# Performance work log

Hardware: AMD Instinct MI355X
Metric: run time of the kernel (lower is better)

## Reference

```python
import jax, jax.numpy as jnp
import numpy as np

VOCAB, HIDDEN, BATCH, T = 32000, 256, 16, 256


def setup_inputs() -> dict:
    key = jax.random.key(0)
    ks = jax.random.split(key, 8)
    s_in = 1.0 / np.sqrt(HIDDEN)  # torch nn.RNN init scale (1/sqrt(hidden))
    inputs = jax.random.randint(ks[0], (BATCH, T), 0, VOCAB)
    targets = jax.random.randint(ks[1], (BATCH, T), 0, VOCAB)
    # RNN params: torch stores W_ih as (hidden, vocab); we keep the transpose
    # (vocab, hidden) so one_hot(x) @ W_ih.T == Wih[x] (an exact gather).
    Wih = jax.random.uniform(ks[2], (VOCAB, HIDDEN), minval=-s_in, maxval=s_in)
    bih = jax.random.uniform(ks[3], (HIDDEN,), minval=-s_in, maxval=s_in)
    Whh = jax.random.uniform(ks[4], (HIDDEN, HIDDEN), minval=-s_in, maxval=s_in)
    bhh = jax.random.uniform(ks[5], (HIDDEN,), minval=-s_in, maxval=s_in)
    Wfc = jax.random.uniform(ks[6], (VOCAB, HIDDEN), minval=-s_in, maxval=s_in)
    bfc = jax.random.uniform(ks[7], (VOCAB,), minval=-s_in, maxval=s_in)
    return {"inputs": inputs, "targets": targets, "Wih": Wih, "bih": bih,
            "Whh": Whh, "bhh": bhh, "Wfc": Wfc, "bfc": bfc}


def reference(inputs, targets, Wih, bih, Whh, bhh, Wfc, bfc):
    # one_hot(inputs) @ W_ih.T + b_ih  ==  Wih[inputs] + bih (exact same math)
    xproj = Wih[inputs] + bih                      # (B, T, H)
    B = inputs.shape[0]
    h0 = jnp.zeros((B, HIDDEN), dtype=Wih.dtype)

    def step(h, xt):
        h = jnp.tanh(xt + h @ Whh.T + bhh)
        return h, h

    _, hs = jax.lax.scan(step, h0, jnp.swapaxes(xproj, 0, 1))  # (T, B, H)
    hs = jnp.swapaxes(hs, 0, 1)                    # (B, T, H)
    logits = hs @ Wfc.T + bfc                      # (B, T, V)
    logp = jax.nn.log_softmax(logits, axis=-1)
    nll = -jnp.take_along_axis(logp, targets[..., None], axis=-1)
    return jnp.mean(nll)                           # scalar cross-entropy loss
```

## Files before the change

kernel.cpp:

```cpp
#include <hip/hip_runtime.h>
#include <hip/hip_bf16.h>
#include <stdint.h>

#define VOCAB 32000
#define HID   256
#define BATCH 16
#define SEQT  256
#define ROWS  (BATCH*SEQT)

typedef __attribute__((ext_vector_type(8))) short bf16x8_t;
typedef __attribute__((ext_vector_type(4))) float f32x4_t;

__device__ __forceinline__ short f2bs(float x) {
    __hip_bfloat16 h = __float2bfloat16(x);
    return *reinterpret_cast<short*>(&h);
}
__device__ __forceinline__ bf16x8_t cvt8(float4 a, float4 b) {
    union { short s[8]; bf16x8_t v; } u;
    u.s[0] = f2bs(a.x); u.s[1] = f2bs(a.y); u.s[2] = f2bs(a.z); u.s[3] = f2bs(a.w);
    u.s[4] = f2bs(b.x); u.s[5] = f2bs(b.y); u.s[6] = f2bs(b.z); u.s[7] = f2bs(b.w);
    return u.v;
}
__device__ __forceinline__ void barrier_lds() {
    asm volatile("s_waitcnt lgkmcnt(0)\n\ts_barrier" ::: "memory");
}
__device__ __forceinline__ float tanh_exp(float x) {
    float e = __builtin_amdgcn_exp2f(x * 2.885390081777927f);
    return fmaf(-2.f, __builtin_amdgcn_rcpf(e + 1.f), 1.f);
}
__device__ __forceinline__ uint32_t pk_bf16(float lo, float hi) {
    uint32_t r;
    asm("v_cvt_pk_bf16_f32 %0, %1, %2" : "=v"(r) : "v"(lo), "v"(hi));
    return r;
}


__global__ __launch_bounds__(256) void xproj_kernel(
    const int* __restrict__ inputs,
    const float* __restrict__ Wih,
    const float* __restrict__ bih,
    const float* __restrict__ bhh,
    const float* __restrict__ Wfc,
    float* __restrict__ xp,
    float* __restrict__ S,
    __hip_bfloat16* __restrict__ Wfcb,
    int do_cvt)
{
    int idx = blockIdx.x * 256 + threadIdx.x;
    int h  = idx & 255;
    int tb = idx >> 8;
    int b  = tb & 15;
    int t  = tb >> 4;
    int id = inputs[b * SEQT + t];
    xp[idx] = Wih[(size_t)id * HID + h] + bih[h] + bhh[h];
    if (idx < ROWS) S[idx] = 0.0f;
    if (do_cvt && idx < (VOCAB * HID / 8)) {
        const float4* p = (const float4*)(Wfc + (size_t)idx * 8);
        int n  = idx >> 5;
        int c  = idx & 31;
        int ki = c >> 2;
        int lh = c & 3;
        size_t dst = (size_t)(n >> 4) * 4096 + ki * 512 + lh * 128 + (n & 15) * 8;
        *(bf16x8_t*)((short*)Wfcb + dst) = cvt8(p[0], p[1]);
    }
}

__global__ __launch_bounds__(512, 1) void rnn_kernel(
    const float* __restrict__ xp,
    const float* __restrict__ Whh,
    __hip_bfloat16* __restrict__ hs)
{
    __shared__ short hbuf[2][16][264];
    const int tid = threadIdx.x;
    const int l = tid & 63, w = tid >> 6;
    const int lr = l & 15, lh = l >> 4;
    const int cm = tid >> 5;
    const int cc = (tid & 31) * 8;
    const int n0 = w * 32 + lr * 2;
    const int cpoff = ((cc >> 5) * 512) + (((cc >> 3) & 3) * 128) + cm * 8;

    bf16x8_t bfrag[2][8];
#pragma unroll
    for (int nt = 0; nt < 2; nt++) {
#pragma unroll
        for (int ki = 0; ki < 8; ki++) {
            const float4* p = (const float4*)(Whh + (size_t)(n0 + nt) * HID + ki * 32 + lh * 8);
            bfrag[nt][ki] = cvt8(p[0], p[1]);
        }
    }
    for (int i = tid; i < 16 * 264; i += 512) ((short*)hbuf[0])[i] = 0;
    __syncthreads();

    float2 xva[4], xvb[4];
#pragma unroll
    for (int r = 0; r < 4; r++)
        xva[r] = *(const float2*)(xp + (lh * 4 + r) * HID + n0);

    auto step = [&](int SRC, int DST, float2* xv, float2* xn, int t) {
        if (t > 0) {
            bf16x8_t hv = *(const bf16x8_t*)(&hbuf[SRC][cm][cc]);
            *(bf16x8_t*)((short*)hs + (size_t)(t - 1) * 4096 + cpoff) = hv;
        }
        bf16x8_t afr[8];
#pragma unroll
        for (int ki = 0; ki < 8; ki++)
            afr[ki] = *(const bf16x8_t*)(&hbuf[SRC][lr][ki * 32 + lh * 8]);

        f32x4_t a0a = {xv[0].x, xv[1].x, xv[2].x, xv[3].x};
        f32x4_t a1a = {xv[0].y, xv[1].y, xv[2].y, xv[3].y};
        f32x4_t a0b = {0.f, 0.f, 0.f, 0.f};
        f32x4_t a1b = {0.f, 0.f, 0.f, 0.f};
#pragma unroll
        for (int ki = 0; ki < 4; ki++) {
            a0a = __builtin_amdgcn_mfma_f32_16x16x32_bf16(afr[ki],     bfrag[0][ki],     a0a, 0, 0, 0);
            a0b = __builtin_amdgcn_mfma_f32_16x16x32_bf16(afr[ki + 4], bfrag[0][ki + 4], a0b, 0, 0, 0);
            a1a = __builtin_amdgcn_mfma_f32_16x16x32_bf16(afr[ki],     bfrag[1][ki],     a1a, 0, 0, 0);
            a1b = __builtin_amdgcn_mfma_f32_16x16x32_bf16(afr[ki + 4], bfrag[1][ki + 4], a1b, 0, 0, 0);
        }

        if (t + 1 < SEQT) {
            const float* xb = xp + (size_t)(t + 1) * (BATCH * HID);
#pragma unroll
            for (int r = 0; r < 4; r++)
                xn[r] = *(const float2*)(xb + (lh * 4 + r) * HID + n0);
        }

#pragma unroll
        for (int r = 0; r < 4; r++) {
            float v0 = a0a[r] + a0b[r];
            float v1 = a1a[r] + a1b[r];
            uint32_t pk = pk_bf16(tanh_exp(v0), tanh_exp(v1));
            *(uint32_t*)(&hbuf[DST][lh * 4 + r][n0]) = pk;
        }
        barrier_lds();
    };

    for (int t = 0; t < SEQT; t += 2) {
        step(0, 1, xva, xvb, t);
        step(1, 0, xvb, xva, t + 1);
    }
    bf16x8_t hv = *(const bf16x8_t*)(&hbuf[0][cm][cc]);
    *(bf16x8_t*)((short*)hs + (size_t)(SEQT - 1) * 4096 + cpoff) = hv;
}

template <bool BF16B>
__global__ __launch_bounds__(256) void fc_kernel(
    const __hip_bfloat16* __restrict__ hsz,
    const void* __restrict__ WfcP,
    const float* __restrict__ bfc,
    const int* __restrict__ targets,
    float* __restrict__ S,
    float* __restrict__ TL)
{
    __shared__ int tgt[128];

    const int bid = blockIdx.x;
    const int xcd = bid & 7;
    const int j   = bid >> 3;
    const int m_id = j & 31;
    const int n_id = (j >> 5) * 8 + xcd;
    if (n_id >= VOCAB / 128) return;
    const int m0 = m_id * 128, n0 = n_id * 128;

    const int tid = threadIdx.x;
    const int l = tid & 63, w = tid >> 6;
    const int lr = l & 15, lh = l >> 4;
    const int wm = (w >> 1) * 64, wn = (w & 1) * 64;

    if (tid < 128) {
        int r = m0 + tid;
        tgt[tid] = targets[((r & 15) << 8) | (r >> 4)];
    }

    const short* Ab = (const short*)hsz +
        ((size_t)(m_id * 8 + (wm >> 4)) * 8) * 512 + l * 8;
    const short* Bb = (const short*)WfcP +
        ((size_t)(n_id * 8 + (wn >> 4)) * 8) * 512 + l * 8;
    const float* Bf = (const float*)WfcP;

    f32x4_t acc[4][4];
    const f32x4_t z = {0.f, 0.f, 0.f, 0.f};
#pragma unroll
    for (int i = 0; i < 4; i++)
#pragma unroll
        for (int jj = 0; jj < 4; jj++) acc[i][jj] = z;

    bf16x8_t a[2][4], b[2][4];
    auto loadA = [&](int buf, int ki) {
#pragma unroll
        for (int mt = 0; mt < 4; mt++)
            a[buf][mt] = *(const bf16x8_t*)(Ab + mt * 4096 + ki * 512);
    };
    auto loadB = [&](int buf, int ki) {
#pragma unroll
        for (int nt = 0; nt < 4; nt++) {
            if (BF16B) {
                b[buf][nt] = *(const bf16x8_t*)(Bb + nt * 4096 + ki * 512);
            } else {
                int n = n0 + wn + nt * 16 + lr;
                const float4* p = (const float4*)(Bf + (size_t)n * HID + ki * 32 + lh * 8);
                b[buf][nt] = cvt8(p[0], p[1]);
            }
        }
    };

    loadA(0, 0); loadB(0, 0);
#pragma unroll
    for (int ki = 0; ki < 8; ki++) {
        const int cur = ki & 1;
        if (ki < 7) { loadA(cur ^ 1, ki + 1); loadB(cur ^ 1, ki + 1); }
#pragma unroll
        for (int mt = 0; mt < 4; mt++)
#pragma unroll
            for (int nt = 0; nt < 4; nt++)
                acc[mt][nt] = __builtin_amdgcn_mfma_f32_16x16x32_bf16(
                    a[cur][mt], b[cur][nt], acc[mt][nt], 0, 0, 0);
    }
    __syncthreads();

    int tg[16];
#pragma unroll
    for (int i = 0; i < 16; i++)
        tg[i] = tgt[wm + (i >> 2) * 16 + lh * 4 + (i & 3)];

    float rsum[16];
#pragma unroll
    for (int i = 0; i < 16; i++) rsum[i] = 0.f;
#pragma unroll
    for (int nt = 0; nt < 4; nt++) {
        int n = n0 + wn + nt * 16 + lr;
        float bias = bfc[n];
#pragma unroll
        for (int mt = 0; mt < 4; mt++)
#pragma unroll
            for (int r = 0; r < 4; r++) {
                float v = acc[mt][nt][r] + bias;
                rsum[mt * 4 + r] += __expf(v);
                if (tg[mt * 4 + r] == n)
                    TL[m0 + wm + mt * 16 + lh * 4 + r] = v;
            }
    }
#pragma unroll
    for (int m = 1; m < 16; m <<= 1)
#pragma unroll
        for (int i = 0; i < 16; i++) rsum[i] += __shfl_xor(rsum[i], m, 64);
    if (lr == 0) {
#pragma unroll
        for (int i = 0; i < 16; i++) {
            int r = m0 + wm + (i >> 2) * 16 + lh * 4 + (i & 3);
            atomicAdd(&S[r], rsum[i]);
        }
    }
}

__global__ __launch_bounds__(256) void loss_kernel(
    const float* __restrict__ S,
    const float* __restrict__ TL,
    float* __restrict__ out)
{
    int tid = threadIdx.x;
    float p = 0.f;
    for (int i = tid; i < ROWS; i += 256) p += __logf(S[i]) - TL[i];
#pragma unroll
    for (int m = 1; m < 64; m <<= 1) p += __shfl_xor(p, m, 64);
    __shared__ float red[4];
    if ((tid & 63) == 0) red[tid >> 6] = p;
    __syncthreads();
    if (tid == 0)
        out[0] = (red[0] + red[1] + red[2] + red[3]) / (float)ROWS;
}

extern "C" void kernel_launch(void* const* d_in, const int* in_sizes, int n_in,
                              void* d_out, int out_size, void* d_ws, size_t ws_size,
                              hipStream_t stream)
{
    (void)in_sizes; (void)n_in; (void)out_size;
    const int*   inputs  = (const int*)d_in[0];
    const int*   targets = (const int*)d_in[1];
    const float* Wih = (const float*)d_in[2];
    const float* bih = (const float*)d_in[3];
    const float* Whh = (const float*)d_in[4];
    const float* bhh = (const float*)d_in[5];
    const float* Wfc = (const float*)d_in[6];
    const float* bfc = (const float*)d_in[7];

    float* S  = (float*)d_ws;
    float* TL = S + ROWS;
    float* xp = TL + ROWS;
    __hip_bfloat16* hs = (__hip_bfloat16*)(xp + (size_t)SEQT * BATCH * HID);
    __hip_bfloat16* Wfcb = hs + (size_t)ROWS * HID;

    const size_t need = (size_t)(2 * ROWS) * 4 + (size_t)ROWS * HID * 4
                      + (size_t)ROWS * HID * 2 + (size_t)VOCAB * HID * 2;
    const int use_bf16b = (ws_size >= need) ? 1 : 0;

    xproj_kernel<<<(SEQT * BATCH * HID) / 256, 256, 0, stream>>>(
        inputs, Wih, bih, bhh, Wfc, xp, S, Wfcb, use_bf16b);
    rnn_kernel<<<1, 512, 0, stream>>>(xp, Whh, hs);
    if (use_bf16b)
        fc_kernel<true><<<8192, 256, 0, stream>>>(hs, (const void*)Wfcb, bfc, targets, S, TL);
    else
        fc_kernel<false><<<8192, 256, 0, stream>>>(hs, (const void*)Wfc, bfc, targets, S, TL);
    loss_kernel<<<1, 256, 0, stream>>>(S, TL, (float*)d_out);
}
```

Baseline: 468.0 us.

## Persist A tile in LDS across vocab tiles; shrink RNN to 4 waves with direct hs stores

```diff
diff --git a/kernel.cpp b/kernel.cpp
--- a/kernel.cpp
+++ b/kernel.cpp
@@ -55,96 +55,98 @@
     xp[idx] = Wih[(size_t)id * HID + h] + bih[h] + bhh[h];
     if (idx < ROWS) S[idx] = 0.0f;
     if (do_cvt && idx < (VOCAB * HID / 8)) {
-        const float4* p = (const float4*)(Wfc + (size_t)idx * 8);
-        int n  = idx >> 5;
-        int c  = idx & 31;
-        int ki = c >> 2;
-        int lh = c & 3;
-        size_t dst = (size_t)(n >> 4) * 4096 + ki * 512 + lh * 128 + (n & 15) * 8;
-        *(bf16x8_t*)((short*)Wfcb + dst) = cvt8(p[0], p[1]);
-    }
-}
-
-__global__ __launch_bounds__(512, 1) void rnn_kernel(
+        int e   = idx * 8;
+        int m   = (e >> 3) & 15;
+        int lhh = (e >> 7) & 3;
+        int ki  = (e >> 9) & 7;
+        int tile = e >> 12;
+        const float4* p = (const float4*)(Wfc + (size_t)(tile * 16 + m) * HID
+                                          + ki * 32 + lhh * 8);
+        *(bf16x8_t*)((short*)Wfcb + (size_t)e) = cvt8(p[0], p[1]);
+    }
+}
+
+__global__ __launch_bounds__(256, 1) void rnn_kernel(
     const float* __restrict__ xp,
     const float* __restrict__ Whh,
     __hip_bfloat16* __restrict__ hs)
 {
-    __shared__ short hbuf[2][16][264];
+    __shared__ __align__(16) short hbuf[2][16][264];
     const int tid = threadIdx.x;
     const int l = tid & 63, w = tid >> 6;
     const int lr = l & 15, lh = l >> 4;
-    const int cm = tid >> 5;
-    const int cc = (tid & 31) * 8;
-    const int n0 = w * 32 + lr * 2;
-    const int cpoff = ((cc >> 5) * 512) + (((cc >> 3) & 3) * 128) + cm * 8;
-
-    bf16x8_t bfrag[2][8];
-#pragma unroll
-    for (int nt = 0; nt < 2; nt++) {
+    const int n0 = w * 64 + lr * 4;
+    short* hsg = (short*)hs + ((n0 >> 5) * 512) + (((n0 >> 3) & 3) * 128) + (n0 & 7);
+
+    bf16x8_t bfrag[4][8];
+#pragma unroll
+    for (int c = 0; c < 4; c++)
 #pragma unroll
         for (int ki = 0; ki < 8; ki++) {
-            const float4* p = (const float4*)(Whh + (size_t)(n0 + nt) * HID + ki * 32 + lh * 8);
-            bfrag[nt][ki] = cvt8(p[0], p[1]);
-        }
-    }
-    for (int i = tid; i < 16 * 264; i += 512) ((short*)hbuf[0])[i] = 0;
+            const float4* p = (const float4*)(Whh + (size_t)(n0 + c) * HID + ki * 32 + lh * 8);
+            bfrag[c][ki] = cvt8(p[0], p[1]);
+        }
+    for (int i = tid; i < 16 * 264; i += 256) ((short*)hbuf[0])[i] = 0;
     __syncthreads();
 
-    float2 xva[4], xvb[4];
+    float4 xv[4], xw[4];
 #pragma unroll
     for (int r = 0; r < 4; r++)
-        xva[r] = *(const float2*)(xp + (lh * 4 + r) * HID + n0);
-
-    auto step = [&](int SRC, int DST, float2* xv, float2* xn, int t) {
-        if (t > 0) {
-            bf16x8_t hv = *(const bf16x8_t*)(&hbuf[SRC][cm][cc]);
-            *(bf16x8_t*)((short*)hs + (size_t)(t - 1) * 4096 + cpoff) = hv;
-        }
+        xv[r] = *(const float4*)(xp + (lh * 4 + r) * HID + n0);
+
+    auto step = [&](int SRC, int DST, float4* xc, float4* xn, int t) {
         bf16x8_t afr[8];
 #pragma unroll
         for (int ki = 0; ki < 8; ki++)
             afr[ki] = *(const bf16x8_t*)(&hbuf[SRC][lr][ki * 32 + lh * 8]);
 
-        f32x4_t a0a = {xv[0].x, xv[1].x, xv[2].x, xv[3].x};
-        f32x4_t a1a = {xv[0].y, xv[1].y, xv[2].y, xv[3].y};
-        f32x4_t a0b = {0.f, 0.f, 0.f, 0.f};
-        f32x4_t a1b = {0.f, 0.f, 0.f, 0.f};
+        f32x4_t A0 = {xc[0].x, xc[1].x, xc[2].x, xc[3].x};
+        f32x4_t A1 = {xc[0].y, xc[1].y, xc[2].y, xc[3].y};
+        f32x4_t A2 = {xc[0].z, xc[1].z, xc[2].z, xc[3].z};
+        f32x4_t A3 = {xc[0].w, xc[1].w, xc[2].w, xc[3].w};
+        f32x4_t B0 = {0,0,0,0}, B1 = {0,0,0,0}, B2 = {0,0,0,0}, B3 = {0,0,0,0};
 #pragma unroll
         for (int ki = 0; ki < 4; ki++) {
-            a0a = __builtin_amdgcn_mfma_f32_16x16x32_bf16(afr[ki],     bfrag[0][ki],     a0a, 0, 0, 0);
-            a0b = __builtin_amdgcn_mfma_f32_16x16x32_bf16(afr[ki + 4], bfrag[0][ki + 4], a0b, 0, 0, 0);
-            a1a = __builtin_amdgcn_mfma_f32_16x16x32_bf16(afr[ki],     bfrag[1][ki],     a1a, 0, 0, 0);
-            a1b = __builtin_amdgcn_mfma_f32_16x16x32_bf16(afr[ki + 4], bfrag[1][ki + 4], a1b, 0, 0, 0);
+            A0 = __builtin_amdgcn_mfma_f32_16x16x32_bf16(afr[ki],     bfrag[0][ki],     A0, 0, 0, 0);
+            B0 = __builtin_amdgcn_mfma_f32_16x16x32_bf16(afr[ki + 4], bfrag[0][ki + 4], B0, 0, 0, 0);
+            A1 = __builtin_amdgcn_mfma_f32_16x16x32_bf16(afr[ki],     bfrag[1][ki],     A1, 0, 0, 0);
+            B1 = __builtin_amdgcn_mfma_f32_16x16x32_bf16(afr[ki + 4], bfrag[1][ki + 4], B1, 0, 0, 0);
+            A2 = __builtin_amdgcn_mfma_f32_16x16x32_bf16(afr[ki],     bfrag[2][ki],     A2, 0, 0, 0);
+            B2 = __builtin_amdgcn_mfma_f32_16x16x32_bf16(afr[ki + 4], bfrag[2][ki + 4], B2, 0, 0, 0);
+            A3 = __builtin_amdgcn_mfma_f32_16x16x32_bf16(afr[ki],     bfrag[3][ki],     A3, 0, 0, 0);
+            B3 = __builtin_amdgcn_mfma_f32_16x16x32_bf16(afr[ki + 4], bfrag[3][ki + 4], B3, 0, 0, 0);
         }
 
         if (t + 1 < SEQT) {
             const float* xb = xp + (size_t)(t + 1) * (BATCH * HID);
 #pragma unroll
             for (int r = 0; r < 4; r++)
-                xn[r] = *(const float2*)(xb + (lh * 4 + r) * HID + n0);
+                xn[r] = *(const float4*)(xb + (lh * 4 + r) * HID + n0);
         }
 
 #pragma unroll
         for (int r = 0; r < 4; r++) {
-            float v0 = a0a[r] + a0b[r];
-            float v1 = a1a[r] + a1b[r];
-            uint32_t pk = pk_bf16(tanh_exp(v0), tanh_exp(v1));
-            *(uint32_t*)(&hbuf[DST][lh * 4 + r][n0]) = pk;
+            float v0 = A0[r] + B0[r];
+            float v1 = A1[r] + B1[r];
+            float v2 = A2[r] + B2[r];
+            float v3 = A3[r] + B3[r];
+            uint2 u;
+            u.x = pk_bf16(tanh_exp(v0), tanh_exp(v1));
+            u.y = pk_bf16(tanh_exp(v2), tanh_exp(v3));
+            *(uint2*)(&hbuf[DST][lh * 4 + r][n0]) = u;
+            *(uint2*)(hsg + (size_t)t * 4096 + (lh * 4 + r) * 8) = u;
         }
         barrier_lds();
     };
 
     for (int t = 0; t < SEQT; t += 2) {
-        step(0, 1, xva, xvb, t);
-        step(1, 0, xvb, xva, t + 1);
-    }
-    bf16x8_t hv = *(const bf16x8_t*)(&hbuf[0][cm][cc]);
-    *(bf16x8_t*)((short*)hs + (size_t)(SEQT - 1) * 4096 + cpoff) = hv;
+        step(0, 1, xv, xw, t);
+        step(1, 0, xw, xv, t + 1);
+    }
 }
 
 template <bool BF16B>
-__global__ __launch_bounds__(256) void fc_kernel(
+__global__ __launch_bounds__(256, 2) void fc_kernel(
     const __hip_bfloat16* __restrict__ hsz,
     const void* __restrict__ WfcP,
     const float* __restrict__ bfc,
@@ -152,70 +154,33 @@
     float* __restrict__ S,
     float* __restrict__ TL)
 {
+    __shared__ __align__(16) short As[8 * 4096];
     __shared__ int tgt[128];
 
     const int bid = blockIdx.x;
-    const int xcd = bid & 7;
-    const int j   = bid >> 3;
-    const int m_id = j & 31;
-    const int n_id = (j >> 5) * 8 + xcd;
-    if (n_id >= VOCAB / 128) return;
-    const int m0 = m_id * 128, n0 = n_id * 128;
+    const int x = bid & 7;
+    const int k = bid >> 3;
+    const int g = x + 8 * (k >> 5);
+    const int m_id = k & 31;
+    const int m0 = m_id * 128;
 
     const int tid = threadIdx.x;
     const int l = tid & 63, w = tid >> 6;
     const int lr = l & 15, lh = l >> 4;
     const int wm = (w >> 1) * 64, wn = (w & 1) * 64;
 
+    {
+        const short* src = (const short*)hsz + (size_t)m_id * 32768 + tid * 8;
+#pragma unroll
+        for (int i = 0; i < 16; i++) {
+            bf16x8_t v = *(const bf16x8_t*)(src + i * 2048);
+            *(bf16x8_t*)(As + i * 2048 + tid * 8) = v;
+        }
+    }
     if (tid < 128) {
         int r = m0 + tid;
         tgt[tid] = targets[((r & 15) << 8) | (r >> 4)];
     }
-
-    const short* Ab = (const short*)hsz +
-        ((size_t)(m_id * 8 + (wm >> 4)) * 8) * 512 + l * 8;
-    const short* Bb = (const short*)WfcP +
-        ((size_t)(n_id * 8 + (wn >> 4)) * 8) * 512 + l * 8;
-    const float* Bf = (const float*)WfcP;
-
-    f32x4_t acc[4][4];
-    const f32x4_t z = {0.f, 0.f, 0.f, 0.f};
-#pragma unroll
-    for (int i = 0; i < 4; i++)
-#pragma unroll
-        for (int jj = 0; jj < 4; jj++) acc[i][jj] = z;
-
-    bf16x8_t a[2][4], b[2][4];
-    auto loadA = [&](int buf, int ki) {
-#pragma unroll
-        for (int mt = 0; mt < 4; mt++)
-            a[buf][mt] = *(const bf16x8_t*)(Ab + mt * 4096 + ki * 512);
-    };
-    auto loadB = [&](int buf, int ki) {
-#pragma unroll
-        for (int nt = 0; nt < 4; nt++) {
-            if (BF16B) {
-                b[buf][nt] = *(const bf16x8_t*)(Bb + nt * 4096 + ki * 512);
-            } else {
-                int n = n0 + wn + nt * 16 + lr;
-                const float4* p = (const float4*)(Bf + (size_t)n * HID + ki * 32 + lh * 8);
-                b[buf][nt] = cvt8(p[0], p[1]);
-            }
-        }
-    };
-
-    loadA(0, 0); loadB(0, 0);
-#pragma unroll
-    for (int ki = 0; ki < 8; ki++) {
-        const int cur = ki & 1;
-        if (ki < 7) { loadA(cur ^ 1, ki + 1); loadB(cur ^ 1, ki + 1); }
-#pragma unroll
-        for (int mt = 0; mt < 4; mt++)
-#pragma unroll
-            for (int nt = 0; nt < 4; nt++)
-                acc[mt][nt] = __builtin_amdgcn_mfma_f32_16x16x32_bf16(
-                    a[cur][mt], b[cur][nt], acc[mt][nt], 0, 0, 0);
-    }
     __syncthreads();
 
     int tg[16];
@@ -223,23 +188,84 @@
     for (int i = 0; i < 16; i++)
         tg[i] = tgt[wm + (i >> 2) * 16 + lh * 4 + (i & 3)];
 
+    const short* Asl = As + (wm >> 4) * 4096 + l * 8;
+    const short* Bsw = (const short*)WfcP + (size_t)(wn >> 4) * 4096 + l * 8;
+    const float* Bf  = (const float*)WfcP;
+
+    bf16x8_t aa[2][4], bb[2][4];
+
+#define LOADA(buf_, kk_) {                                                   \
+    _Pragma("unroll")                                                        \
+    for (int mt = 0; mt < 4; mt++)                                           \
+        aa[buf_][mt] = *(const bf16x8_t*)(Asl + mt * 4096 + (kk_) * 512); }
+
+#define LOADB(buf_, s_) {                                                    \
+    int tt_ = (s_) >> 3, kk_ = (s_) & 7;                                     \
+    int nid_ = g * 8 + tt_; if (nid_ >= VOCAB / 128) nid_ = 0;               \
+    if (BF16B) {                                                             \
+        const short* bp_ = Bsw + (size_t)nid_ * 32768 + kk_ * 512;           \
+        _Pragma("unroll")                                                    \
+        for (int nt = 0; nt < 4; nt++)                                       \
+            bb[buf_][nt] = *(const bf16x8_t*)(bp_ + nt * 4096);              \
+    } else {                                                                 \
+        _Pragma("unroll")                                                    \
+        for (int nt = 0; nt < 4; nt++) {                                     \
+            int n_ = nid_ * 128 + wn + nt * 16 + lr;                         \
+            const float4* p_ = (const float4*)(Bf + (size_t)n_ * HID         \
+                                               + kk_ * 32 + lh * 8);         \
+            bb[buf_][nt] = cvt8(p_[0], p_[1]);                               \
+        }                                                                    \
+    } }
+
+    LOADB(0, 0);
+    LOADB(1, 1);
+    LOADA(0, 0);
+
     float rsum[16];
 #pragma unroll
     for (int i = 0; i < 16; i++) rsum[i] = 0.f;
-#pragma unroll
-    for (int nt = 0; nt < 4; nt++) {
-        int n = n0 + wn + nt * 16 + lr;
-        float bias = bfc[n];
-#pragma unroll
-        for (int mt = 0; mt < 4; mt++)
-#pragma unroll
-            for (int r = 0; r < 4; r++) {
-                float v = acc[mt][nt][r] + bias;
-                rsum[mt * 4 + r] += __expf(v);
-                if (tg[mt * 4 + r] == n)
-                    TL[m0 + wm + mt * 16 + lh * 4 + r] = v;
+
+    for (int t = 0; t < 8; t++) {
+        f32x4_t acc[4][4];
+        const f32x4_t z = {0.f, 0.f, 0.f, 0.f};
+#pragma unroll
+        for (int i = 0; i < 4; i++)
+#pragma unroll
+            for (int jj = 0; jj < 4; jj++) acc[i][jj] = z;
+
+#pragma unroll
+        for (int ki = 0; ki < 8; ki++) {
+            LOADA((ki + 1) & 1, (ki + 1) & 7);
+#pragma unroll
+            for (int mt = 0; mt < 4; mt++)
+#pragma unroll
+                for (int nt = 0; nt < 4; nt++)
+                    acc[mt][nt] = __builtin_amdgcn_mfma_f32_16x16x32_bf16(
+                        aa[ki & 1][mt], bb[ki & 1][nt], acc[mt][nt], 0, 0, 0);
+            if (t * 8 + ki + 2 < 64) LOADB(ki & 1, t * 8 + ki + 2);
+        }
+
+        int nid = g * 8 + t;
+        if (nid < VOCAB / 128) {
+#pragma unroll
+            for (int nt = 0; nt < 4; nt++) {
+                int n = nid * 128 + wn + nt * 16 + lr;
+                float bias = bfc[n];
+#pragma unroll
+                for (int mt = 0; mt < 4; mt++)
+#pragma unroll
+                    for (int r = 0; r < 4; r++) {
+                        float v = acc[mt][nt][r] + bias;
+                        rsum[mt * 4 + r] += __expf(v);
+                        if (tg[mt * 4 + r] == n)
+                            TL[m0 + wm + mt * 16 + lh * 4 + r] = v;
+                    }
             }
-    }
+        }
+    }
+#undef LOADA
+#undef LOADB
+
 #pragma unroll
     for (int m = 1; m < 16; m <<= 1)
 #pragma unroll
@@ -296,10 +322,10 @@
 
     xproj_kernel<<<(SEQT * BATCH * HID) / 256, 256, 0, stream>>>(
         inputs, Wih, bih, bhh, Wfc, xp, S, Wfcb, use_bf16b);
-    rnn_kernel<<<1, 512, 0, stream>>>(xp, Whh, hs);
+    rnn_kernel<<<1, 256, 0, stream>>>(xp, Whh, hs);
     if (use_bf16b)
-        fc_kernel<true><<<8192, 256, 0, stream>>>(hs, (const void*)Wfcb, bfc, targets, S, TL);
+        fc_kernel<true><<<1024, 256, 0, stream>>>(hs, (const void*)Wfcb, bfc, targets, S, TL);
     else
-        fc_kernel<false><<<8192, 256, 0, stream>>>(hs, (const void*)Wfc, bfc, targets, S, TL);
+        fc_kernel<false><<<1024, 256, 0, stream>>>(hs, (const void*)Wfc, bfc, targets, S, TL);
     loss_kernel<<<1, 256, 0, stream>>>(S, TL, (float*)d_out);
 }
```

Result: slower. 900.2 us (+92.4%).
